# Optimization experiments

Measured on AMD Instinct MI355X. Metric: run time of the kernel, lower is better.

Reference implementation:

```python
import jax, jax.numpy as jnp
import numpy as np

DIM = 128
N = 8192
E = 262144
EPS = 1e-8  # torch.cosine_similarity eps


def setup_inputs() -> dict:
    key = jax.random.key(0)
    k1, k2, k3, k4 = jax.random.split(key, 4)
    x = jax.random.normal(k1, (N, DIM), dtype=jnp.float32)
    edge_index = jax.random.randint(k2, (2, E), 0, N, dtype=jnp.int32)
    # GCNConv parameters: linear weight (glorot-ish) and bias
    W_gcn = jax.random.normal(k3, (DIM, DIM), dtype=jnp.float32) / np.sqrt(DIM)
    b_gcn = jnp.zeros((DIM,), dtype=jnp.float32)
    return {"x": x, "edge_index": edge_index, "W_gcn": W_gcn, "b_gcn": b_gcn}


def _cosine_attention(x):
    # torch.cosine_similarity(x.unsqueeze(1), x.unsqueeze(0), dim=-1)
    # == (x @ x.T) / max(||x_i|| * ||x_j||, eps)
    nrm = jnp.sqrt(jnp.sum(x * x, axis=-1))                      # [N]
    denom = jnp.maximum(nrm[:, None] * nrm[None, :], EPS)        # [N, N]
    sim = (x @ x.T) / denom                                      # [N, N]
    return jax.nn.sigmoid(sim @ x)                               # [N, dim]


def _gcn_conv(x, edge_index, W, b):
    n = x.shape[0]
    xw = x @ W                                                   # [N, dim]
    # add self-loops
    loops = jnp.arange(n, dtype=edge_index.dtype)
    row = jnp.concatenate([edge_index[0], loops])                # source
    col = jnp.concatenate([edge_index[1], loops])                # target
    # symmetric normalization: deg computed on target nodes
    deg = jax.ops.segment_sum(jnp.ones_like(col, dtype=x.dtype), col, num_segments=n)
    dis = jnp.where(deg > 0, jax.lax.rsqrt(jnp.maximum(deg, 1.0)), 0.0)
    dis = jnp.where(deg > 0, deg ** -0.5, 0.0)
    norm = dis[row] * dis[col]                                   # [E+N]
    msgs = xw[row] * norm[:, None]                               # [E+N, dim]
    out = jax.ops.segment_sum(msgs, col, num_segments=n)         # [N, dim]
    return out + b


def reference(x, edge_index, W_gcn, b_gcn):
    att = _cosine_attention(x)
    g = _gcn_conv(x, edge_index, W_gcn, b_gcn)
    return g * att
```

## Files before the change

### kernel.cpp

```cpp
#include <hip/hip_runtime.h>
#include <math.h>

#define NN   8192
#define DIM  128
#define NE   262144
#define XU   64
#define JCH  128
#define HBH  64
#define HEB  (NE / HBH)
#define PBP  64
#define PEB  (NE / PBP)
#define GU   128
#define GR   64

typedef __attribute__((ext_vector_type(8))) short bf16x8;
typedef __attribute__((ext_vector_type(4))) float f32x4;

static __device__ __forceinline__ unsigned short f2bf(float f) {
  unsigned int u = __float_as_uint(f);
  return (unsigned short)((u + 0x7FFFu + ((u >> 16) & 1u)) >> 16);
}
static __device__ __forceinline__ float bf2f(unsigned int h) {
  return __uint_as_float(h << 16);
}
static __device__ __forceinline__ unsigned int pk2(float a, float b) {
  return (unsigned int)f2bf(a) | ((unsigned int)f2bf(b) << 16);
}


static __device__ void ph_xtx(int u, int tid, char* smem,
    const float* __restrict__ x, float* __restrict__ rinv,
    float* __restrict__ Mpart) {
  char* XTs = smem;
  char* XTu = smem + 32768;
  int j0 = u * JCH;
  int jl = tid >> 1, half = tid & 1;
  const float4* xr = (const float4*)(x + (size_t)(j0 + jl) * DIM + half * 64);
  float ss = 0.f;
  #pragma unroll
  for (int i = 0; i < 16; ++i) {
    float4 v = xr[i];
    ss += v.x * v.x + v.y * v.y + v.z * v.z + v.w * v.w;
  }
  ss += __shfl_xor(ss, 1);
  float rv = 1.0f / sqrtf(ss);
  if (half == 0) rinv[j0 + jl] = rv;
  #pragma unroll
  for (int c4 = 0; c4 < 16; ++c4) {
    float4 v = xr[c4];
    #pragma unroll
    for (int i = 0; i < 4; ++i) {
      int d = half * 64 + c4 * 4 + i;
      float f = ((const float*)&v)[i];
      int off = d * 256 + ((jl * 2) ^ ((d & 7) << 4));
      *(unsigned short*)(XTs + off) = f2bf(f * rv);
      *(unsigned short*)(XTu + off) = f2bf(f);
    }
  }
  __syncthreads();

  int w = tid >> 6, lane = tid & 63;
  int l15 = lane & 15, g16 = (lane >> 4) * 16, swz = (lane & 7) << 4;
  f32x4 acc[2][8];
  #pragma unroll
  for (int dt = 0; dt < 2; ++dt)
    #pragma unroll
    for (int ct = 0; ct < 8; ++ct) acc[dt][ct] = (f32x4){0.f, 0.f, 0.f, 0.f};
  #pragma unroll
  for (int ks = 0; ks < 4; ++ks) {
    int ko = (ks * 64 + g16) ^ swz;
    bf16x8 a0 = *(const bf16x8*)(XTs + (w * 32 + l15) * 256 + ko);
    bf16x8 a1 = *(const bf16x8*)(XTs + (w * 32 + 16 + l15) * 256 + ko);
    #pragma unroll
    for (int ct = 0; ct < 8; ++ct) {
      bf16x8 b = *(const bf16x8*)(XTu + (ct * 16 + l15) * 256 + ko);
      acc[0][ct] = __builtin_amdgcn_mfma_f32_16x16x32_bf16(a0, b, acc[0][ct], 0, 0, 0);
      acc[1][ct] = __builtin_amdgcn_mfma_f32_16x16x32_bf16(a1, b, acc[1][ct], 0, 0, 0);
    }
  }
  float* o = Mpart + (size_t)u * (DIM * DIM);
  #pragma unroll
  for (int dt = 0; dt < 2; ++dt)
    #pragma unroll
    for (int ct = 0; ct < 8; ++ct)
      #pragma unroll
      for (int r = 0; r < 4; ++r) {
        int row = w * 32 + dt * 16 + (lane >> 4) * 4 + r;
        int col = ct * 16 + l15;
        o[row * DIM + col] = acc[dt][ct][r];
      }
}

static __device__ void ph_hist(int h, int tid, int* ldeg,
    const int* __restrict__ ei, int* __restrict__ gcnt, int* __restrict__ slot) {
  int4* lz = (int4*)ldeg;
  #pragma unroll
  for (int i = tid; i < NN / 4; i += 256) lz[i] = make_int4(0, 0, 0, 0);
  __syncthreads();
  int e0 = h * HEB + tid * 16;
  int4 c0 = *(const int4*)(ei + NE + e0);
  int4 c1 = *(const int4*)(ei + NE + e0 + 4);
  int4 c2 = *(const int4*)(ei + NE + e0 + 8);
  int4 c3 = *(const int4*)(ei + NE + e0 + 12);
  int r0  = atomicAdd(&ldeg[c0.x], 1);
  int r1  = atomicAdd(&ldeg[c0.y], 1);
  int r2  = atomicAdd(&ldeg[c0.z], 1);
  int r3  = atomicAdd(&ldeg[c0.w], 1);
  int r4  = atomicAdd(&ldeg[c1.x], 1);
  int r5  = atomicAdd(&ldeg[c1.y], 1);
  int r6  = atomicAdd(&ldeg[c1.z], 1);
  int r7  = atomicAdd(&ldeg[c1.w], 1);
  int r8  = atomicAdd(&ldeg[c2.x], 1);
  int r9  = atomicAdd(&ldeg[c2.y], 1);
  int r10 = atomicAdd(&ldeg[c2.z], 1);
  int r11 = atomicAdd(&ldeg[c2.w], 1);
  int r12 = atomicAdd(&ldeg[c3.x], 1);
  int r13 = atomicAdd(&ldeg[c3.y], 1);
  int r14 = atomicAdd(&ldeg[c3.z], 1);
  int r15 = atomicAdd(&ldeg[c3.w], 1);
  __syncthreads();
  int binb = tid * 32;
  #pragma unroll
  for (int i = 0; i < 8; ++i) {
    int4 v = *(int4*)&ldeg[binb + i * 4];
    if (v.x) ldeg[binb + i * 4 + 0] = atomicAdd(&gcnt[binb + i * 4 + 0], v.x);
    if (v.y) ldeg[binb + i * 4 + 1] = atomicAdd(&gcnt[binb + i * 4 + 1], v.y);
    if (v.z) ldeg[binb + i * 4 + 2] = atomicAdd(&gcnt[binb + i * 4 + 2], v.z);
    if (v.w) ldeg[binb + i * 4 + 3] = atomicAdd(&gcnt[binb + i * 4 + 3], v.w);
  }
  __syncthreads();
  int4 s0 = make_int4(ldeg[c0.x] + r0,  ldeg[c0.y] + r1,  ldeg[c0.z] + r2,  ldeg[c0.w] + r3);
  int4 s1 = make_int4(ldeg[c1.x] + r4,  ldeg[c1.y] + r5,  ldeg[c1.z] + r6,  ldeg[c1.w] + r7);
  int4 s2 = make_int4(ldeg[c2.x] + r8,  ldeg[c2.y] + r9,  ldeg[c2.z] + r10, ldeg[c2.w] + r11);
  int4 s3 = make_int4(ldeg[c3.x] + r12, ldeg[c3.y] + r13, ldeg[c3.z] + r14, ldeg[c3.w] + r15);
  *(int4*)(slot + e0)      = s0;
  *(int4*)(slot + e0 + 4)  = s1;
  *(int4*)(slot + e0 + 8)  = s2;
  *(int4*)(slot + e0 + 12) = s3;
}

static __device__ void ph_mred(int u, int tid, float* smemf,
    const float* __restrict__ Mpart, unsigned short* __restrict__ Bg) {
  int j0 = u * 64;
  int jj = tid & 63, sub = tid >> 6;
  const float* mp = Mpart + (size_t)(sub * 16) * (DIM * DIM) + j0;
  float s = 0.f;
  #pragma unroll 4
  for (int k = 0; k < 16; ++k) s += mp[(size_t)k * (DIM * DIM) + jj];
  smemf[sub * 64 + jj] = s;
  __syncthreads();
  if (tid < 64) {
    float v = smemf[tid] + smemf[64 + tid] + smemf[128 + tid] + smemf[192 + tid];
    int flat = j0 + tid;
    int row = flat >> 7, col = flat & 127;
    Bg[(size_t)(128 + row) * DIM + col] = f2bf(v);
  }
}

static __device__ void ph_wt(int b, int tid, float* smemf,
    const float* __restrict__ W, unsigned short* __restrict__ Bg) {
  float4* dst = (float4*)smemf;
  const float4* src = (const float4*)(W + (size_t)b * 32 * DIM);
  #pragma unroll
  for (int i = 0; i < 4; ++i) dst[tid + 256 * i] = src[tid + 256 * i];
  __syncthreads();
  int j = tid >> 1, kh = (tid & 1) * 16;
  uint4 p0, p1;
  p0.x = pk2(smemf[(kh + 0) * DIM + j],  smemf[(kh + 1) * DIM + j]);
  p0.y = pk2(smemf[(kh + 2) * DIM + j],  smemf[(kh + 3) * DIM + j]);
  p0.z = pk2(smemf[(kh + 4) * DIM + j],  smemf[(kh + 5) * DIM + j]);
  p0.w = pk2(smemf[(kh + 6) * DIM + j],  smemf[(kh + 7) * DIM + j]);
  p1.x = pk2(smemf[(kh + 8) * DIM + j],  smemf[(kh + 9) * DIM + j]);
  p1.y = pk2(smemf[(kh + 10) * DIM + j], smemf[(kh + 11) * DIM + j]);
  p1.z = pk2(smemf[(kh + 12) * DIM + j], smemf[(kh + 13) * DIM + j]);
  p1.w = pk2(smemf[(kh + 14) * DIM + j], smemf[(kh + 15) * DIM + j]);
  uint4* op = (uint4*)(Bg + (size_t)j * DIM + b * 32 + kh);
  op[0] = p0; op[1] = p1;
}

static __device__ void ph_scan(int tid, int* wsum,
    const int* __restrict__ gcnt, int* __restrict__ offs, float* __restrict__ dis) {
  int lane = tid & 63, wave = tid >> 6;
  const int4* g4 = (const int4*)gcnt;
  int s = 0;
  #pragma unroll
  for (int i = 0; i < 8; ++i) { int4 v = g4[tid * 8 + i]; s += v.x + v.y + v.z + v.w; }
  int sc = s;
  #pragma unroll
  for (int off = 1; off < 64; off <<= 1) {
    int v = __shfl_up(sc, off);
    if (lane >= off) sc += v;
  }
  if (lane == 63) wsum[wave] = sc;
  __syncthreads();
  if (wave == 0 && lane < 4) {
    int v = wsum[lane];
    #pragma unroll
    for (int off = 1; off < 4; off <<= 1) {
      int u = __shfl_up(v, off);
      if (lane >= off) v += u;
    }
    wsum[lane] = v;
  }
  __syncthreads();
  int run = (wave ? wsum[wave - 1] : 0) + sc - s;
  #pragma unroll
  for (int i = 0; i < 8; ++i) {
    int4 v = g4[tid * 8 + i];
    int4 o;
    o.x = run; run += v.x;
    o.y = run; run += v.y;
    o.z = run; run += v.z;
    o.w = run; run += v.w;
    *(int4*)&offs[tid * 32 + i * 4] = o;
    float4 d;
    d.x = rsqrtf((float)(v.x + 1)); d.y = rsqrtf((float)(v.y + 1));
    d.z = rsqrtf((float)(v.z + 1)); d.w = rsqrtf((float)(v.w + 1));
    *(float4*)&dis[tid * 32 + i * 4] = d;
  }
}

static __device__ void ph_gemm(int u, int tid, char* smem,
    const float* __restrict__ x, const unsigned short* __restrict__ Bg,
    const float* __restrict__ rinv, const float* __restrict__ dis,
    unsigned short* __restrict__ xws, float* __restrict__ att) {
  char* A = smem;
  float* rvs = (float*)(smem + 16384);
  float* dss = rvs + 64;
  int row0 = u * GR;
  #pragma unroll
  for (int i = 0; i < 4; ++i) {
    int c = tid + 256 * i;
    int row = c >> 4, kc = c & 15;
    const float4* s = (const float4*)(x + (size_t)(row0 + row) * DIM + kc * 8);
    float4 v0 = s[0], v1 = s[1];
    uint4 p;
    p.x = pk2(v0.x, v0.y); p.y = pk2(v0.z, v0.w);
    p.z = pk2(v1.x, v1.y); p.w = pk2(v1.z, v1.w);
    *(uint4*)(A + row * 256 + ((kc * 16) ^ ((row & 7) << 4))) = p;
  }
  if (tid < 64) { rvs[tid] = rinv[row0 + tid]; dss[tid] = dis[row0 + tid]; }

  int w = tid >> 6, lane = tid & 63;
  int l15 = lane & 15, g16 = (lane >> 4) * 16, swz = (lane & 7) << 4;
  bf16x8 breg[4][4];
  const char* Bgb = (const char*)Bg;
  #pragma unroll
  for (int ct = 0; ct < 4; ++ct) {
    int j = w * 64 + ct * 16 + l15;
    #pragma unroll
    for (int ks = 0; ks < 4; ++ks)
      breg[ct][ks] = *(const bf16x8*)(Bgb + j * 256 + ks * 64 + g16);
  }
  __syncthreads();

  f32x4 acc[4][4];
  #pragma unroll
  for (int rt = 0; rt < 4; ++rt)
    #pragma unroll
    for (int ct = 0; ct < 4; ++ct) acc[rt][ct] = (f32x4){0.f, 0.f, 0.f, 0.f};
  #pragma unroll
  for (int rt = 0; rt < 4; ++rt) {
    #pragma unroll
    for (int ks = 0; ks < 4; ++ks) {
      bf16x8 a = *(const bf16x8*)(A + (rt * 16 + l15) * 256 + ((ks * 64 + g16) ^ swz));
      #pragma unroll
      for (int ct = 0; ct < 4; ++ct)
        acc[rt][ct] = __builtin_amdgcn_mfma_f32_16x16x32_bf16(a, breg[ct][ks], acc[rt][ct], 0, 0, 0);
    }
  }

  bool isW = (w < 2);
  #pragma unroll
  for (int rt = 0; rt < 4; ++rt)
    #pragma unroll
    for (int ct = 0; ct < 4; ++ct)
      #pragma unroll
      for (int r = 0; r < 4; ++r) {
        int rl = rt * 16 + (lane >> 4) * 4 + r;
        int row = row0 + rl;
        int col = w * 64 + ct * 16 + l15;
        float v = acc[rt][ct][r];
        if (isW) {
          xws[(size_t)row * DIM + col] = f2bf(v * dss[rl]);
        } else {
          float gv = 1.0f / (1.0f + __expf(-v * rvs[rl]));
          att[(size_t)row * DIM + (col - 128)] = gv;
        }
      }
}

static __device__ void ph_place(int u, int tid,
    const int* __restrict__ ei, const int* __restrict__ offs,
    const int* __restrict__ slot, int* __restrict__ sorted) {
  int e0 = u * PEB + tid * 16;
  #pragma unroll
  for (int i = 0; i < 4; ++i) {
    int4 sv = *(const int4*)(ei + e0 + i * 4);
    int4 cv = *(const int4*)(ei + NE + e0 + i * 4);
    int4 sl = *(const int4*)(slot + e0 + i * 4);
    sorted[offs[cv.x] + sl.x] = sv.x;
    sorted[offs[cv.y] + sl.y] = sv.y;
    sorted[offs[cv.z] + sl.z] = sv.z;
    sorted[offs[cv.w] + sl.w] = sv.w;
  }
}

__global__ __launch_bounds__(256) void k_pA(const float* __restrict__ x,
    const int* __restrict__ ei, float* __restrict__ rinv,
    float* __restrict__ Mpart, int* __restrict__ gcnt, int* __restrict__ slot) {
  __shared__ float smem[16512];
  int u = blockIdx.x, tid = threadIdx.x;
  if (u < XU) ph_xtx(u, tid, (char*)smem, x, rinv, Mpart);
  else        ph_hist(u - XU, tid, (int*)smem, ei, gcnt, slot);
}
__global__ __launch_bounds__(256) void k_pB(const float* __restrict__ Mpart,
    const float* __restrict__ W, unsigned short* __restrict__ Bg,
    const int* __restrict__ gcnt, int* __restrict__ offs, float* __restrict__ dis) {
  __shared__ float smem[4224];
  int u = blockIdx.x, tid = threadIdx.x;
  if (u < 256)      ph_mred(u, tid, smem, Mpart, Bg);
  else if (u == 256) ph_scan(tid, (int*)smem, gcnt, offs, dis);
  else              ph_wt(u - 257, tid, smem, W, Bg);
}
__global__ __launch_bounds__(256) void k_pC(const float* __restrict__ x,
    const unsigned short* __restrict__ Bg, const float* __restrict__ rinv,
    const float* __restrict__ dis, const int* __restrict__ ei,
    const int* __restrict__ offs, const int* __restrict__ slot,
    int* __restrict__ sorted, unsigned short* __restrict__ xws,
    float* __restrict__ att) {
  __shared__ float smem[4224];
  int u = blockIdx.x, tid = threadIdx.x;
  if (u < GU) ph_gemm(u, tid, (char*)smem, x, Bg, rinv, dis, xws, att);
  else        ph_place(u - GU, tid, ei, offs, slot, sorted);
}
__global__ __launch_bounds__(64) void k_pD(const int* __restrict__ offs,
    const int* __restrict__ gcnt, const float* __restrict__ dis,
    const unsigned short* __restrict__ xws, const float* __restrict__ att,
    const float* __restrict__ bias, const int* __restrict__ sorted,
    float* __restrict__ out) {
  int c = blockIdx.x, t = threadIdx.x;
  int base = offs[c];
  int cnt  = gcnt[c];
  const unsigned int* xw2 = (const unsigned int*)xws;
  unsigned int sv = xw2[(size_t)c * 64 + t];
  float acc0 = bf2f(sv & 0xffffu), acc1 = bf2f(sv >> 16);
  int k = 0;
  for (; k + 8 <= cnt; k += 8) {
    int4 i0 = *(const int4*)(sorted + base + k);
    int4 i1 = *(const int4*)(sorted + base + k + 4);
    unsigned int v0 = xw2[(size_t)i0.x * 64 + t];
    unsigned int v1 = xw2[(size_t)i0.y * 64 + t];
    unsigned int v2 = xw2[(size_t)i0.z * 64 + t];
    unsigned int v3 = xw2[(size_t)i0.w * 64 + t];
    unsigned int v4 = xw2[(size_t)i1.x * 64 + t];
    unsigned int v5 = xw2[(size_t)i1.y * 64 + t];
    unsigned int v6 = xw2[(size_t)i1.z * 64 + t];
    unsigned int v7 = xw2[(size_t)i1.w * 64 + t];
    acc0 += bf2f(v0 & 0xffffu) + bf2f(v1 & 0xffffu) + bf2f(v2 & 0xffffu) + bf2f(v3 & 0xffffu)
          + bf2f(v4 & 0xffffu) + bf2f(v5 & 0xffffu) + bf2f(v6 & 0xffffu) + bf2f(v7 & 0xffffu);
    acc1 += bf2f(v0 >> 16) + bf2f(v1 >> 16) + bf2f(v2 >> 16) + bf2f(v3 >> 16)
          + bf2f(v4 >> 16) + bf2f(v5 >> 16) + bf2f(v6 >> 16) + bf2f(v7 >> 16);
  }
  for (; k + 4 <= cnt; k += 4) {
    int4 i0 = *(const int4*)(sorted + base + k);
    unsigned int v0 = xw2[(size_t)i0.x * 64 + t];
    unsigned int v1 = xw2[(size_t)i0.y * 64 + t];
    unsigned int v2 = xw2[(size_t)i0.z * 64 + t];
    unsigned int v3 = xw2[(size_t)i0.w * 64 + t];
    acc0 += bf2f(v0 & 0xffffu) + bf2f(v1 & 0xffffu) + bf2f(v2 & 0xffffu) + bf2f(v3 & 0xffffu);
    acc1 += bf2f(v0 >> 16) + bf2f(v1 >> 16) + bf2f(v2 >> 16) + bf2f(v3 >> 16);
  }
  for (; k < cnt; ++k) {
    unsigned int v = xw2[(size_t)sorted[base + k] * 64 + t];
    acc0 += bf2f(v & 0xffffu);
    acc1 += bf2f(v >> 16);
  }
  float dc = dis[c];
  float2 at = ((const float2*)att)[(size_t)c * 64 + t];
  float2 bs = ((const float2*)bias)[t];
  float2 o;
  o.x = (acc0 * dc + bs.x) * at.x;
  o.y = (acc1 * dc + bs.y) * at.y;
  ((float2*)out)[(size_t)c * 64 + t] = o;
}

extern "C" void kernel_launch(void* const* d_in, const int* in_sizes, int n_in,
                              void* d_out, int out_size, void* d_ws, size_t ws_size,
                              hipStream_t stream) {
  const float* x  = (const float*)d_in[0];
  const int*   ei = (const int*)  d_in[1];
  const float* W  = (const float*)d_in[2];
  const float* b  = (const float*)d_in[3];
  float* out = (float*)d_out;

  unsigned short* xws = (unsigned short*)d_ws;
  float* att   = (float*)(xws + (size_t)NN * DIM);
  unsigned short* Bg = (unsigned short*)(att + (size_t)NN * DIM);
  float* Mpart = (float*)(Bg + 256 * DIM);
  float* rinv  = Mpart + (size_t)XU * DIM * DIM;
  float* dis   = rinv + NN;
  int*   gcnt  = (int*)(dis + NN);
  int*   offs  = gcnt + NN;
  int*   slot  = offs + NN;
  int*   sorted= slot + NE;

  hipMemsetAsync(gcnt, 0, NN * sizeof(int), stream);

  k_pA<<<XU + HBH, 256, 0, stream>>>(x, ei, rinv, Mpart, gcnt, slot);
  k_pB<<<261, 256, 0, stream>>>(Mpart, W, Bg, gcnt, offs, dis);
  k_pC<<<GU + PBP, 256, 0, stream>>>(x, Bg, rinv, dis, ei, offs, slot, sorted,
                                     xws, att);
  k_pD<<<NN, 64, 0, stream>>>(offs, gcnt, dis, xws, att, b, sorted, out);
}
```

Baseline: 106.1 us.

## Merge reduce/scan and gemm/place phases into one kernel with atomic-counter spin sync

Moves the W transpose phase into the first kernel and fuses the former k_pB and k_pC launches into a single kernel. The gemm and place blocks spin on a global atomic counter until all 257 reduce/scan blocks finish, and they prefetch their inputs before waiting. This removes one kernel launch and its inter-kernel drain gap. It relies on the producer blocks being scheduled before or alongside the waiting blocks (lower block indices, 2 blocks per CU allowed), so there is a deadlock risk if residency is insufficient.

Result: slower. 162.9 us (+53.6%).

```diff
diff --git a/kernel.cpp b/kernel.cpp
--- a/kernel.cpp
+++ b/kernel.cpp
@@ -12,6 +12,7 @@
 #define PEB  (NE / PBP)
 #define GU   128
 #define GR   64
+#define DONE_TARGET 257
 
 typedef __attribute__((ext_vector_type(8))) short bf16x8;
 typedef __attribute__((ext_vector_type(4))) float f32x4;
@@ -223,7 +224,8 @@
 static __device__ void ph_gemm(int u, int tid, char* smem,
     const float* __restrict__ x, const unsigned short* __restrict__ Bg,
     const float* __restrict__ rinv, const float* __restrict__ dis,
-    unsigned short* __restrict__ xws, float* __restrict__ att) {
+    const int* __restrict__ sync, unsigned short* __restrict__ xws,
+    float* __restrict__ att) {
   char* A = smem;
   float* rvs = (float*)(smem + 16384);
   float* dss = rvs + 64;
@@ -239,6 +241,11 @@
     p.z = pk2(v1.x, v1.y); p.w = pk2(v1.z, v1.w);
     *(uint4*)(A + row * 256 + ((kc * 16) ^ ((row & 7) << 4))) = p;
   }
+  if (tid == 0) {
+    while (__hip_atomic_load(&sync[0], __ATOMIC_ACQUIRE, __HIP_MEMORY_SCOPE_AGENT) < DONE_TARGET)
+      __builtin_amdgcn_s_sleep(2);
+  }
+  __syncthreads();
   if (tid < 64) { rvs[tid] = rinv[row0 + tid]; dss[tid] = dis[row0 + tid]; }
 
   int w = tid >> 6, lane = tid & 63;
@@ -292,47 +299,63 @@
 
 static __device__ void ph_place(int u, int tid,
     const int* __restrict__ ei, const int* __restrict__ offs,
-    const int* __restrict__ slot, int* __restrict__ sorted) {
+    const int* __restrict__ slot, const int* __restrict__ sync,
+    int* __restrict__ sorted) {
   int e0 = u * PEB + tid * 16;
+  int4 sv[4], cv[4], sl[4];
   #pragma unroll
   for (int i = 0; i < 4; ++i) {
-    int4 sv = *(const int4*)(ei + e0 + i * 4);
-    int4 cv = *(const int4*)(ei + NE + e0 + i * 4);
-    int4 sl = *(const int4*)(slot + e0 + i * 4);
-    sorted[offs[cv.x] + sl.x] = sv.x;
-    sorted[offs[cv.y] + sl.y] = sv.y;
-    sorted[offs[cv.z] + sl.z] = sv.z;
-    sorted[offs[cv.w] + sl.w] = sv.w;
+    sv[i] = *(const int4*)(ei + e0 + i * 4);
+    cv[i] = *(const int4*)(ei + NE + e0 + i * 4);
+    sl[i] = *(const int4*)(slot + e0 + i * 4);
+  }
+  if (tid == 0) {
+    while (__hip_atomic_load(&sync[0], __ATOMIC_ACQUIRE, __HIP_MEMORY_SCOPE_AGENT) < DONE_TARGET)
+      __builtin_amdgcn_s_sleep(2);
+  }
+  __syncthreads();
+  #pragma unroll
+  for (int i = 0; i < 4; ++i) {
+    sorted[offs[cv[i].x] + sl[i].x] = sv[i].x;
+    sorted[offs[cv[i].y] + sl[i].y] = sv[i].y;
+    sorted[offs[cv[i].z] + sl[i].z] = sv[i].z;
+    sorted[offs[cv[i].w] + sl[i].w] = sv[i].w;
   }
 }
 
 __global__ __launch_bounds__(256) void k_pA(const float* __restrict__ x,
-    const int* __restrict__ ei, float* __restrict__ rinv,
-    float* __restrict__ Mpart, int* __restrict__ gcnt, int* __restrict__ slot) {
+    const int* __restrict__ ei, const float* __restrict__ W,
+    float* __restrict__ rinv, float* __restrict__ Mpart,
+    int* __restrict__ gcnt, int* __restrict__ slot,
+    unsigned short* __restrict__ Bg) {
   __shared__ float smem[16512];
   int u = blockIdx.x, tid = threadIdx.x;
-  if (u < XU) ph_xtx(u, tid, (char*)smem, x, rinv, Mpart);
-  else        ph_hist(u - XU, tid, (int*)smem, ei, gcnt, slot);
-}
-__global__ __launch_bounds__(256) void k_pB(const float* __restrict__ Mpart,
-    const float* __restrict__ W, unsigned short* __restrict__ Bg,
-    const int* __restrict__ gcnt, int* __restrict__ offs, float* __restrict__ dis) {
+  if (u < XU)            ph_xtx(u, tid, (char*)smem, x, rinv, Mpart);
+  else if (u < XU + HBH) ph_hist(u - XU, tid, (int*)smem, ei, gcnt, slot);
+  else                   ph_wt(u - XU - HBH, tid, smem, W, Bg);
+}
+__global__ __launch_bounds__(256, 2) void k_pBC(const float* __restrict__ Mpart,
+    const float* __restrict__ x, unsigned short* __restrict__ Bg,
+    const int* __restrict__ gcnt, int* __restrict__ offs, float* __restrict__ dis,
+    const float* __restrict__ rinv, const int* __restrict__ ei,
+    const int* __restrict__ slot, int* __restrict__ sorted,
+    unsigned short* __restrict__ xws, float* __restrict__ att,
+    int* __restrict__ sync) {
   __shared__ float smem[4224];
   int u = blockIdx.x, tid = threadIdx.x;
-  if (u < 256)      ph_mred(u, tid, smem, Mpart, Bg);
-  else if (u == 256) ph_scan(tid, (int*)smem, gcnt, offs, dis);
-  else              ph_wt(u - 257, tid, smem, W, Bg);
-}
-__global__ __launch_bounds__(256) void k_pC(const float* __restrict__ x,
-    const unsigned short* __restrict__ Bg, const float* __restrict__ rinv,
-    const float* __restrict__ dis, const int* __restrict__ ei,
-    const int* __restrict__ offs, const int* __restrict__ slot,
-    int* __restrict__ sorted, unsigned short* __restrict__ xws,
-    float* __restrict__ att) {
-  __shared__ float smem[4224];
-  int u = blockIdx.x, tid = threadIdx.x;
-  if (u < GU) ph_gemm(u, tid, (char*)smem, x, Bg, rinv, dis, xws, att);
-  else        ph_place(u - GU, tid, ei, offs, slot, sorted);
+  if (u < 256) {
+    ph_mred(u, tid, smem, Mpart, Bg);
+    __threadfence(); __syncthreads();
+    if (tid == 0) atomicAdd(sync, 1);
+  } else if (u == 256) {
+    ph_scan(tid, (int*)smem, gcnt, offs, dis);
+    __threadfence(); __syncthreads();
+    if (tid == 0) atomicAdd(sync, 1);
+  } else if (u < 257 + GU) {
+    ph_gemm(u - 257, tid, (char*)smem, x, Bg, rinv, dis, sync, xws, att);
+  } else {
+    ph_place(u - 257 - GU, tid, ei, offs, slot, sync, sorted);
+  }
 }
 __global__ __launch_bounds__(64) void k_pD(const int* __restrict__ offs,
     const int* __restrict__ gcnt, const float* __restrict__ dis,
@@ -401,15 +424,15 @@
   float* rinv  = Mpart + (size_t)XU * DIM * DIM;
   float* dis   = rinv + NN;
   int*   gcnt  = (int*)(dis + NN);
-  int*   offs  = gcnt + NN;
+  int*   sync  = gcnt + NN;
+  int*   offs  = sync + 4;
   int*   slot  = offs + NN;
   int*   sorted= slot + NE;
 
-  hipMemsetAsync(gcnt, 0, NN * sizeof(int), stream);
-
-  k_pA<<<XU + HBH, 256, 0, stream>>>(x, ei, rinv, Mpart, gcnt, slot);
-  k_pB<<<261, 256, 0, stream>>>(Mpart, W, Bg, gcnt, offs, dis);
-  k_pC<<<GU + PBP, 256, 0, stream>>>(x, Bg, rinv, dis, ei, offs, slot, sorted,
-                                     xws, att);
+  hipMemsetAsync(gcnt, 0, (NN + 4) * sizeof(int), stream);
+
+  k_pA<<<XU + HBH + 4, 256, 0, stream>>>(x, ei, W, rinv, Mpart, gcnt, slot, Bg);
+  k_pBC<<<257 + GU + PBP, 256, 0, stream>>>(Mpart, x, Bg, gcnt, offs, dis, rinv,
+                                            ei, slot, sorted, xws, att, sync);
   k_pD<<<NN, 64, 0, stream>>>(offs, gcnt, dis, xws, att, b, sorted, out);
 }
```

## Merge phases: atomic fixed-point XᵀX accumulation and fixed-stride edge buckets

Applied to the files above, without the earlier changes.

The partial XᵀX tiles are now accumulated straight into one shared matrix with fixed-point integer atomics, which drops the Mpart buffer and its reduction kernel. The degree histogram now writes source indices into fixed 96-slot per-node buckets, which removes the prefix scan and the separate placement pass. Degree normalisation is recomputed inline with rsqrt. Launches go from four kernels to three, cutting inter-kernel syncs and global traffic. The cost is fixed-point rounding error in M and silent bucket overflow for any node with in-degree above 96.

Measured after the change: 106.2 us. About the same (+0.1%).

```diff
diff --git a/kernel.cpp b/kernel.cpp
--- a/kernel.cpp
+++ b/kernel.cpp
@@ -8,10 +8,11 @@
 #define JCH  128
 #define HBH  64
 #define HEB  (NE / HBH)
-#define PBP  64
-#define PEB  (NE / PBP)
 #define GU   128
 #define GR   64
+#define SD   96
+#define MSCALE 1048576.0f
+#define MINV  (1.0f / 1048576.0f)
 
 typedef __attribute__((ext_vector_type(8))) short bf16x8;
 typedef __attribute__((ext_vector_type(4))) float f32x4;
@@ -30,7 +31,7 @@
 
 static __device__ void ph_xtx(int u, int tid, char* smem,
     const float* __restrict__ x, float* __restrict__ rinv,
-    float* __restrict__ Mpart) {
+    int* __restrict__ Mi) {
   char* XTs = smem;
   char* XTu = smem + 32768;
   int j0 = u * JCH;
@@ -78,7 +79,6 @@
       acc[1][ct] = __builtin_amdgcn_mfma_f32_16x16x32_bf16(a1, b, acc[1][ct], 0, 0, 0);
     }
   }
-  float* o = Mpart + (size_t)u * (DIM * DIM);
   #pragma unroll
   for (int dt = 0; dt < 2; ++dt)
     #pragma unroll
@@ -87,12 +87,14 @@
       for (int r = 0; r < 4; ++r) {
         int row = w * 32 + dt * 16 + (lane >> 4) * 4 + r;
         int col = ct * 16 + l15;
-        o[row * DIM + col] = acc[dt][ct][r];
+        atomicAdd(&Mi[row * DIM + col],
+                  __float2int_rn(acc[dt][ct][r] * MSCALE));
       }
 }
 
-static __device__ void ph_hist(int h, int tid, int* ldeg,
-    const int* __restrict__ ei, int* __restrict__ gcnt, int* __restrict__ slot) {
+static __device__ void ph_histplace(int h, int tid, int* ldeg,
+    const int* __restrict__ ei, int* __restrict__ gcnt,
+    int* __restrict__ sorted) {
   int4* lz = (int4*)ldeg;
   #pragma unroll
   for (int i = tid; i < NN / 4; i += 256) lz[i] = make_int4(0, 0, 0, 0);
@@ -102,6 +104,10 @@
   int4 c1 = *(const int4*)(ei + NE + e0 + 4);
   int4 c2 = *(const int4*)(ei + NE + e0 + 8);
   int4 c3 = *(const int4*)(ei + NE + e0 + 12);
+  int4 s0 = *(const int4*)(ei + e0);
+  int4 s1 = *(const int4*)(ei + e0 + 4);
+  int4 s2 = *(const int4*)(ei + e0 + 8);
+  int4 s3 = *(const int4*)(ei + e0 + 12);
   int r0  = atomicAdd(&ldeg[c0.x], 1);
   int r1  = atomicAdd(&ldeg[c0.y], 1);
   int r2  = atomicAdd(&ldeg[c0.z], 1);
@@ -129,32 +135,22 @@
     if (v.w) ldeg[binb + i * 4 + 3] = atomicAdd(&gcnt[binb + i * 4 + 3], v.w);
   }
   __syncthreads();
-  int4 s0 = make_int4(ldeg[c0.x] + r0,  ldeg[c0.y] + r1,  ldeg[c0.z] + r2,  ldeg[c0.w] + r3);
-  int4 s1 = make_int4(ldeg[c1.x] + r4,  ldeg[c1.y] + r5,  ldeg[c1.z] + r6,  ldeg[c1.w] + r7);
-  int4 s2 = make_int4(ldeg[c2.x] + r8,  ldeg[c2.y] + r9,  ldeg[c2.z] + r10, ldeg[c2.w] + r11);
-  int4 s3 = make_int4(ldeg[c3.x] + r12, ldeg[c3.y] + r13, ldeg[c3.z] + r14, ldeg[c3.w] + r15);
-  *(int4*)(slot + e0)      = s0;
-  *(int4*)(slot + e0 + 4)  = s1;
-  *(int4*)(slot + e0 + 8)  = s2;
-  *(int4*)(slot + e0 + 12) = s3;
-}
-
-static __device__ void ph_mred(int u, int tid, float* smemf,
-    const float* __restrict__ Mpart, unsigned short* __restrict__ Bg) {
-  int j0 = u * 64;
-  int jj = tid & 63, sub = tid >> 6;
-  const float* mp = Mpart + (size_t)(sub * 16) * (DIM * DIM) + j0;
-  float s = 0.f;
-  #pragma unroll 4
-  for (int k = 0; k < 16; ++k) s += mp[(size_t)k * (DIM * DIM) + jj];
-  smemf[sub * 64 + jj] = s;
-  __syncthreads();
-  if (tid < 64) {
-    float v = smemf[tid] + smemf[64 + tid] + smemf[128 + tid] + smemf[192 + tid];
-    int flat = j0 + tid;
-    int row = flat >> 7, col = flat & 127;
-    Bg[(size_t)(128 + row) * DIM + col] = f2bf(v);
-  }
+  sorted[c0.x * SD + ldeg[c0.x] + r0]  = s0.x;
+  sorted[c0.y * SD + ldeg[c0.y] + r1]  = s0.y;
+  sorted[c0.z * SD + ldeg[c0.z] + r2]  = s0.z;
+  sorted[c0.w * SD + ldeg[c0.w] + r3]  = s0.w;
+  sorted[c1.x * SD + ldeg[c1.x] + r4]  = s1.x;
+  sorted[c1.y * SD + ldeg[c1.y] + r5]  = s1.y;
+  sorted[c1.z * SD + ldeg[c1.z] + r6]  = s1.z;
+  sorted[c1.w * SD + ldeg[c1.w] + r7]  = s1.w;
+  sorted[c2.x * SD + ldeg[c2.x] + r8]  = s2.x;
+  sorted[c2.y * SD + ldeg[c2.y] + r9]  = s2.y;
+  sorted[c2.z * SD + ldeg[c2.z] + r10] = s2.z;
+  sorted[c2.w * SD + ldeg[c2.w] + r11] = s2.w;
+  sorted[c3.x * SD + ldeg[c3.x] + r12] = s3.x;
+  sorted[c3.y * SD + ldeg[c3.y] + r13] = s3.y;
+  sorted[c3.z * SD + ldeg[c3.z] + r14] = s3.z;
+  sorted[c3.w * SD + ldeg[c3.w] + r15] = s3.w;
 }
 
 static __device__ void ph_wt(int b, int tid, float* smemf,
@@ -178,52 +174,11 @@
   op[0] = p0; op[1] = p1;
 }
 
-static __device__ void ph_scan(int tid, int* wsum,
-    const int* __restrict__ gcnt, int* __restrict__ offs, float* __restrict__ dis) {
-  int lane = tid & 63, wave = tid >> 6;
-  const int4* g4 = (const int4*)gcnt;
-  int s = 0;
-  #pragma unroll
-  for (int i = 0; i < 8; ++i) { int4 v = g4[tid * 8 + i]; s += v.x + v.y + v.z + v.w; }
-  int sc = s;
-  #pragma unroll
-  for (int off = 1; off < 64; off <<= 1) {
-    int v = __shfl_up(sc, off);
-    if (lane >= off) sc += v;
-  }
-  if (lane == 63) wsum[wave] = sc;
-  __syncthreads();
-  if (wave == 0 && lane < 4) {
-    int v = wsum[lane];
-    #pragma unroll
-    for (int off = 1; off < 4; off <<= 1) {
-      int u = __shfl_up(v, off);
-      if (lane >= off) v += u;
-    }
-    wsum[lane] = v;
-  }
-  __syncthreads();
-  int run = (wave ? wsum[wave - 1] : 0) + sc - s;
-  #pragma unroll
-  for (int i = 0; i < 8; ++i) {
-    int4 v = g4[tid * 8 + i];
-    int4 o;
-    o.x = run; run += v.x;
-    o.y = run; run += v.y;
-    o.z = run; run += v.z;
-    o.w = run; run += v.w;
-    *(int4*)&offs[tid * 32 + i * 4] = o;
-    float4 d;
-    d.x = rsqrtf((float)(v.x + 1)); d.y = rsqrtf((float)(v.y + 1));
-    d.z = rsqrtf((float)(v.z + 1)); d.w = rsqrtf((float)(v.w + 1));
-    *(float4*)&dis[tid * 32 + i * 4] = d;
-  }
-}
-
 static __device__ void ph_gemm(int u, int tid, char* smem,
     const float* __restrict__ x, const unsigned short* __restrict__ Bg,
-    const float* __restrict__ rinv, const float* __restrict__ dis,
-    unsigned short* __restrict__ xws, float* __restrict__ att) {
+    const int* __restrict__ Mi, const float* __restrict__ rinv,
+    const int* __restrict__ gcnt, unsigned short* __restrict__ xws,
+    float* __restrict__ att) {
   char* A = smem;
   float* rvs = (float*)(smem + 16384);
   float* dss = rvs + 64;
@@ -239,18 +194,40 @@
     p.z = pk2(v1.x, v1.y); p.w = pk2(v1.z, v1.w);
     *(uint4*)(A + row * 256 + ((kc * 16) ^ ((row & 7) << 4))) = p;
   }
-  if (tid < 64) { rvs[tid] = rinv[row0 + tid]; dss[tid] = dis[row0 + tid]; }
+  if (tid < 64) {
+    rvs[tid] = rinv[row0 + tid];
+    dss[tid] = rsqrtf((float)(gcnt[row0 + tid] + 1));
+  }
 
   int w = tid >> 6, lane = tid & 63;
   int l15 = lane & 15, g16 = (lane >> 4) * 16, swz = (lane & 7) << 4;
   bf16x8 breg[4][4];
-  const char* Bgb = (const char*)Bg;
-  #pragma unroll
-  for (int ct = 0; ct < 4; ++ct) {
-    int j = w * 64 + ct * 16 + l15;
-    #pragma unroll
-    for (int ks = 0; ks < 4; ++ks)
-      breg[ct][ks] = *(const bf16x8*)(Bgb + j * 256 + ks * 64 + g16);
+  if (w < 2) {
+    const char* Bgb = (const char*)Bg;
+    #pragma unroll
+    for (int ct = 0; ct < 4; ++ct) {
+      int j = w * 64 + ct * 16 + l15;
+      #pragma unroll
+      for (int ks = 0; ks < 4; ++ks)
+        breg[ct][ks] = *(const bf16x8*)(Bgb + j * 256 + ks * 64 + g16);
+    }
+  } else {
+    int ge = (lane >> 4) * 8;
+    #pragma unroll
+    for (int ct = 0; ct < 4; ++ct) {
+      int j = (w - 2) * 64 + ct * 16 + l15;
+      #pragma unroll
+      for (int ks = 0; ks < 4; ++ks) {
+        const int4* mp = (const int4*)(Mi + j * DIM + ks * 32 + ge);
+        int4 q0 = mp[0], q1 = mp[1];
+        union { unsigned int u[4]; bf16x8 v; } uu;
+        uu.u[0] = pk2((float)q0.x * MINV, (float)q0.y * MINV);
+        uu.u[1] = pk2((float)q0.z * MINV, (float)q0.w * MINV);
+        uu.u[2] = pk2((float)q1.x * MINV, (float)q1.y * MINV);
+        uu.u[3] = pk2((float)q1.z * MINV, (float)q1.w * MINV);
+        breg[ct][ks] = uu.v;
+      }
+    }
   }
   __syncthreads();
 
@@ -290,57 +267,30 @@
       }
 }
 
-static __device__ void ph_place(int u, int tid,
-    const int* __restrict__ ei, const int* __restrict__ offs,
-    const int* __restrict__ slot, int* __restrict__ sorted) {
-  int e0 = u * PEB + tid * 16;
-  #pragma unroll
-  for (int i = 0; i < 4; ++i) {
-    int4 sv = *(const int4*)(ei + e0 + i * 4);
-    int4 cv = *(const int4*)(ei + NE + e0 + i * 4);
-    int4 sl = *(const int4*)(slot + e0 + i * 4);
-    sorted[offs[cv.x] + sl.x] = sv.x;
-    sorted[offs[cv.y] + sl.y] = sv.y;
-    sorted[offs[cv.z] + sl.z] = sv.z;
-    sorted[offs[cv.w] + sl.w] = sv.w;
-  }
-}
-
 __global__ __launch_bounds__(256) void k_pA(const float* __restrict__ x,
-    const int* __restrict__ ei, float* __restrict__ rinv,
-    float* __restrict__ Mpart, int* __restrict__ gcnt, int* __restrict__ slot) {
+    const int* __restrict__ ei, const float* __restrict__ W,
+    float* __restrict__ rinv, int* __restrict__ Mi,
+    int* __restrict__ gcnt, int* __restrict__ sorted,
+    unsigned short* __restrict__ Bg) {
   __shared__ float smem[16512];
   int u = blockIdx.x, tid = threadIdx.x;
-  if (u < XU) ph_xtx(u, tid, (char*)smem, x, rinv, Mpart);
-  else        ph_hist(u - XU, tid, (int*)smem, ei, gcnt, slot);
-}
-__global__ __launch_bounds__(256) void k_pB(const float* __restrict__ Mpart,
-    const float* __restrict__ W, unsigned short* __restrict__ Bg,
-    const int* __restrict__ gcnt, int* __restrict__ offs, float* __restrict__ dis) {
+  if (u < XU)            ph_xtx(u, tid, (char*)smem, x, rinv, Mi);
+  else if (u < XU + HBH) ph_histplace(u - XU, tid, (int*)smem, ei, gcnt, sorted);
+  else                   ph_wt(u - XU - HBH, tid, smem, W, Bg);
+}
+__global__ __launch_bounds__(256) void k_pG(const float* __restrict__ x,
+    const unsigned short* __restrict__ Bg, const int* __restrict__ Mi,
+    const float* __restrict__ rinv, const int* __restrict__ gcnt,
+    unsigned short* __restrict__ xws, float* __restrict__ att) {
   __shared__ float smem[4224];
-  int u = blockIdx.x, tid = threadIdx.x;
-  if (u < 256)      ph_mred(u, tid, smem, Mpart, Bg);
-  else if (u == 256) ph_scan(tid, (int*)smem, gcnt, offs, dis);
-  else              ph_wt(u - 257, tid, smem, W, Bg);
-}
-__global__ __launch_bounds__(256) void k_pC(const float* __restrict__ x,
-    const unsigned short* __restrict__ Bg, const float* __restrict__ rinv,
-    const float* __restrict__ dis, const int* __restrict__ ei,
-    const int* __restrict__ offs, const int* __restrict__ slot,
-    int* __restrict__ sorted, unsigned short* __restrict__ xws,
-    float* __restrict__ att) {
-  __shared__ float smem[4224];
-  int u = blockIdx.x, tid = threadIdx.x;
-  if (u < GU) ph_gemm(u, tid, (char*)smem, x, Bg, rinv, dis, xws, att);
-  else        ph_place(u - GU, tid, ei, offs, slot, sorted);
-}
-__global__ __launch_bounds__(64) void k_pD(const int* __restrict__ offs,
-    const int* __restrict__ gcnt, const float* __restrict__ dis,
+  ph_gemm(blockIdx.x, threadIdx.x, (char*)smem, x, Bg, Mi, rinv, gcnt, xws, att);
+}
+__global__ __launch_bounds__(64) void k_pD(const int* __restrict__ gcnt,
     const unsigned short* __restrict__ xws, const float* __restrict__ att,
     const float* __restrict__ bias, const int* __restrict__ sorted,
     float* __restrict__ out) {
   int c = blockIdx.x, t = threadIdx.x;
-  int base = offs[c];
+  int base = c * SD;
   int cnt  = gcnt[c];
   const unsigned int* xw2 = (const unsigned int*)xws;
   unsigned int sv = xw2[(size_t)c * 64 + t];
@@ -376,7 +326,7 @@
     acc0 += bf2f(v & 0xffffu);
     acc1 += bf2f(v >> 16);
   }
-  float dc = dis[c];
+  float dc = rsqrtf((float)(cnt + 1));
   float2 at = ((const float2*)att)[(size_t)c * 64 + t];
   float2 bs = ((const float2*)bias)[t];
   float2 o;
@@ -397,19 +347,14 @@
   unsigned short* xws = (unsigned short*)d_ws;
   float* att   = (float*)(xws + (size_t)NN * DIM);
   unsigned short* Bg = (unsigned short*)(att + (size_t)NN * DIM);
-  float* Mpart = (float*)(Bg + 256 * DIM);
-  float* rinv  = Mpart + (size_t)XU * DIM * DIM;
-  float* dis   = rinv + NN;
-  int*   gcnt  = (int*)(dis + NN);
-  int*   offs  = gcnt + NN;
-  int*   slot  = offs + NN;
-  int*   sorted= slot + NE;
-
-  hipMemsetAsync(gcnt, 0, NN * sizeof(int), stream);
-
-  k_pA<<<XU + HBH, 256, 0, stream>>>(x, ei, rinv, Mpart, gcnt, slot);
-  k_pB<<<261, 256, 0, stream>>>(Mpart, W, Bg, gcnt, offs, dis);
-  k_pC<<<GU + PBP, 256, 0, stream>>>(x, Bg, rinv, dis, ei, offs, slot, sorted,
-                                     xws, att);
-  k_pD<<<NN, 64, 0, stream>>>(offs, gcnt, dis, xws, att, b, sorted, out);
-}
+  int*   Mi    = (int*)(Bg + DIM * DIM);
+  int*   gcnt  = Mi + DIM * DIM;
+  float* rinv  = (float*)(gcnt + NN);
+  int*   sorted= (int*)(rinv + NN);
+
+  (void)hipMemsetAsync(Mi, 0, (DIM * DIM + NN) * sizeof(int), stream);
+
+  k_pA<<<XU + HBH + 4, 256, 0, stream>>>(x, ei, W, rinv, Mi, gcnt, sorted, Bg);
+  k_pG<<<GU, 256, 0, stream>>>(x, Bg, Mi, rinv, gcnt, xws, att);
+  k_pD<<<NN, 64, 0, stream>>>(gcnt, xws, att, b, sorted, out);
+}
```
